# Optimization experiments

Hardware: AMD Instinct MI355X
Metric: run time of the kernel (lower is better)

Reference implementation:

```python
import jax, jax.numpy as jnp
import numpy as np

NB_COMP, LAT_DIM, OUT_DIM, N = 16, 128, 512, 16384


def setup_inputs() -> dict:
    key = jax.random.key(0)
    ks = jax.random.split(key, 8)
    eps = jax.random.normal(ks[0], (N, LAT_DIM), dtype=jnp.float32)
    c = jax.random.randint(ks[1], (N,), 0, NB_COMP, dtype=jnp.int32)
    mu = jax.random.normal(ks[2], (NB_COMP, LAT_DIM), dtype=jnp.float32)
    sigma = jax.random.uniform(ks[3], (NB_COMP, LAT_DIM), dtype=jnp.float32)
    # Kaiming-ish init for the two expert linear layers
    W1 = jax.random.normal(ks[4], (NB_COMP, OUT_DIM, LAT_DIM), dtype=jnp.float32) / np.sqrt(LAT_DIM)
    b1 = jax.random.normal(ks[5], (NB_COMP, OUT_DIM), dtype=jnp.float32) * 0.01
    W2 = jax.random.normal(ks[6], (NB_COMP, OUT_DIM, OUT_DIM), dtype=jnp.float32) / np.sqrt(OUT_DIM)
    b2 = jax.random.normal(ks[7], (NB_COMP, OUT_DIM), dtype=jnp.float32) * 0.01
    return {"n": N, "eps": eps, "c": c, "mu": mu, "sigma": sigma,
            "W1": W1, "b1": b1, "W2": W2, "b2": b2}


def reference(n, eps, c, mu, sigma, W1, b1, W2, b2):
    # Per-sample latent from its component's mean-field variational dist:
    # lat[k] = eps[k] * sigma[c[k]] + mu[c[k]]
    lat = eps * sigma[c] + mu[c]                                  # (n, lat_dim)
    # Run every expert's 2-layer MLP densely, then select per-sample expert.
    hidden = jax.nn.relu(jnp.einsum("nd,chd->cnh", lat, W1) + b1[:, None, :])  # (C, n, H)
    out_all = jnp.einsum("cnh,cwh->cnw", hidden, W2) + b2[:, None, :]          # (C, n, W)
    return out_all[c, jnp.arange(n)]                              # (n, weights_dim)
```

## Files before the change

kernel.cpp:

```cpp
#include <hip/hip_runtime.h>

#define NB 16
#define LD 128
#define OD 512
#define NS 16384
#define NPMAX (NS + NB*128)
#define NMT (NPMAX/128)

typedef __attribute__((ext_vector_type(8))) short short8;
typedef __attribute__((ext_vector_type(4))) float f32x4;

#define WS_OFF     128
#define WS_POFF    256
#define WS_PERM    1024
#define WS_W1B     (128*1024)
#define WS_W2B     (WS_W1B + 2*1024*1024)
#define WS_HID     (WS_W2B + 8*1024*1024)
#define WS_LAT     (WS_HID + 20*1024*1024)

#define GLDS16(g, l) __builtin_amdgcn_global_load_lds( \
    (const __attribute__((address_space(1))) unsigned int*)(g), \
    (__attribute__((address_space(3))) unsigned int*)(l), 16, 0, 0)

static __device__ __forceinline__ unsigned short f2bf(float f) {
  unsigned int u = __float_as_uint(f);
  u += 0x7FFFu + ((u >> 16) & 1u);
  return (unsigned short)(u >> 16);
}

#define SORT_T 1024
#define SORT_CH (NS / SORT_T)
__global__ __launch_bounds__(SORT_T) void k_sort(
    const int* __restrict__ c, int* __restrict__ off, int* __restrict__ poff,
    int* __restrict__ perm) {
  __shared__ int cnt[NB * SORT_T];
  __shared__ int totals[NB];
  __shared__ int ebase[NB];

  const int t = threadIdx.x;
  for (int e = 0; e < NB; ++e) cnt[e * SORT_T + t] = 0;
  __syncthreads();

  int myc[SORT_CH];
  for (int i = 0; i < SORT_CH; ++i) {
    int e = c[t * SORT_CH + i];
    myc[i] = e;
    cnt[e * SORT_T + t]++;
  }
  __syncthreads();

  const int w = t >> 6, l = t & 63;
  {
    int carry = 0;
    for (int chunk = 0; chunk < SORT_T / 64; ++chunk) {
      int idx = chunk * 64 + l;
      int v0 = cnt[w * SORT_T + idx];
      int v = v0;
      for (int d = 1; d < 64; d <<= 1) {
        int n = __shfl_up(v, d);
        if (l >= d) v += n;
      }
      cnt[w * SORT_T + idx] = carry + (v - v0);
      carry += __shfl(v, 63);
    }
    if (l == 0) totals[w] = carry;
  }
  __syncthreads();

  if (t == 0) {
    int o = 0, p = 0;
    for (int e = 0; e < NB; ++e) {
      off[e] = o; poff[e] = p; ebase[e] = o;
      o += totals[e];
      p += ((totals[e] + 127) >> 7) << 7;
    }
    off[NB] = o; poff[NB] = p;
  }
  __syncthreads();

  for (int i = 0; i < SORT_CH; ++i) {
    int e = myc[i];
    int pos = ebase[e] + cnt[e * SORT_T + t]++;
    perm[pos] = t * SORT_CH + i;
  }
}

__global__ void k_conv(const float* __restrict__ W1, const float* __restrict__ W2,
                       unsigned short* __restrict__ W1b, unsigned short* __restrict__ W2b) {
  const int n1 = NB * OD * LD / 4, n2 = NB * OD * OD / 4;
  for (int i = blockIdx.x * blockDim.x + threadIdx.x; i < n1 + n2;
       i += gridDim.x * blockDim.x) {
    float4 v; unsigned short* dst;
    if (i < n1) { v = ((const float4*)W1)[i]; dst = W1b + (size_t)i * 4; }
    else        { v = ((const float4*)W2)[i - n1]; dst = W2b + (size_t)(i - n1) * 4; }
    ushort4 o = make_ushort4(f2bf(v.x), f2bf(v.y), f2bf(v.z), f2bf(v.w));
    *(ushort4*)dst = o;
  }
}

__global__ __launch_bounds__(256) void k_lat(
    const float* __restrict__ eps, const float* __restrict__ mu,
    const float* __restrict__ sigma,
    const int* __restrict__ off, const int* __restrict__ poff,
    const int* __restrict__ perm, unsigned short* __restrict__ lat) {
  const int p0 = blockIdx.x * 8;
  if (p0 >= poff[NB]) return;
  int e = 0;
  while (e < NB - 1 && poff[e + 1] <= p0) e++;
  const int off_e = off[e], cnt = off[e + 1] - off_e;
  const int t = threadIdx.x;
  const int p = p0 + (t >> 5), col = (t & 31) * 4;
  const int lrow = p - poff[e];
  ushort4 o;
  if (lrow < cnt) {
    int src = perm[off_e + lrow];
    float4 v  = *(const float4*)(eps + (size_t)src * LD + col);
    float4 sg = *(const float4*)(sigma + e * LD + col);
    float4 m  = *(const float4*)(mu + e * LD + col);
    o = make_ushort4(f2bf(v.x * sg.x + m.x), f2bf(v.y * sg.y + m.y),
                     f2bf(v.z * sg.z + m.z), f2bf(v.w * sg.w + m.w));
  } else {
    o = make_ushort4(0, 0, 0, 0);
  }
  *(ushort4*)(lat + (size_t)p * LD + col) = o;
}

__global__ __launch_bounds__(256) void k_gemm1(
    const float* __restrict__ b1, const unsigned short* __restrict__ W1b,
    const unsigned short* __restrict__ lat,
    const int* __restrict__ poff, unsigned short* __restrict__ hidden) {
  __shared__ alignas(16) unsigned short As[128 * 64];
  __shared__ alignas(16) unsigned short Bs[128 * 64];

  const int mt = blockIdx.y, ct = blockIdx.x;
  const int pr0 = mt * 128;
  if (pr0 >= poff[NB]) return;
  int e = 0;
  while (e < NB - 1 && poff[e + 1] <= pr0) e++;

  const int t = threadIdx.x, w = t >> 6, lane = t & 63;
  const int wr = w >> 1, wc = w & 1;
  const int fr = lane & 15, fg = lane >> 4;
  const int srow = lane >> 3, scol = (lane & 7) * 8;

  f32x4 acc[4][4] = {};
  for (int kt = 0; kt < 2; ++kt) {
#pragma unroll
    for (int i = 0; i < 4; ++i) {
      const int ci = w * 4 + i;
      const int row = ci * 8 + srow;
      GLDS16(lat + (size_t)(pr0 + row) * LD + kt * 64 + scol, As + ci * 512);
      GLDS16(W1b + ((size_t)e * OD + ct * 128 + row) * LD + kt * 64 + scol, Bs + ci * 512);
    }
    __syncthreads();
#pragma unroll
    for (int ks = 0; ks < 2; ++ks) {
      short8 a[4], b[4];
#pragma unroll
      for (int fm = 0; fm < 4; ++fm)
        a[fm] = *(const short8*)(As + (wr * 64 + fm * 16 + fr) * 64 + ks * 32 + fg * 8);
#pragma unroll
      for (int fn = 0; fn < 4; ++fn)
        b[fn] = *(const short8*)(Bs + (wc * 64 + fn * 16 + fr) * 64 + ks * 32 + fg * 8);
#pragma unroll
      for (int fm = 0; fm < 4; ++fm)
#pragma unroll
        for (int fn = 0; fn < 4; ++fn)
          acc[fm][fn] = __builtin_amdgcn_mfma_f32_16x16x32_bf16(a[fm], b[fn], acc[fm][fn], 0, 0, 0);
    }
    __syncthreads();
  }

  const int colb = ct * 128 + wc * 64;
  float bias[4];
#pragma unroll
  for (int fn = 0; fn < 4; ++fn) bias[fn] = b1[e * OD + colb + fn * 16 + fr];
#pragma unroll
  for (int fm = 0; fm < 4; ++fm) {
    const int row0 = pr0 + wr * 64 + fm * 16 + fg * 4;
#pragma unroll
    for (int j = 0; j < 4; ++j) {
      unsigned short* hrow = hidden + (size_t)(row0 + j) * OD + colb;
#pragma unroll
      for (int fn = 0; fn < 4; ++fn)
        hrow[fn * 16 + fr] = f2bf(fmaxf(acc[fm][fn][j] + bias[fn], 0.f));
    }
  }
}

__global__ __launch_bounds__(256) void k_gemm2(
    const float* __restrict__ b2, const unsigned short* __restrict__ W2b,
    const unsigned short* __restrict__ hidden,
    const int* __restrict__ off, const int* __restrict__ poff,
    const int* __restrict__ perm, float* __restrict__ out) {
  __shared__ alignas(16) unsigned short As[128 * 64];
  __shared__ alignas(16) unsigned short Bs[128 * 64];

  const int mt = blockIdx.y, ct = blockIdx.x;
  const int pr0 = mt * 128;
  if (pr0 >= poff[NB]) return;
  int e = 0;
  while (e < NB - 1 && poff[e + 1] <= pr0) e++;
  const int off_e = off[e];
  const int cnt   = off[e + 1] - off_e;
  const int l0    = pr0 - poff[e];

  const int t = threadIdx.x, w = t >> 6, lane = t & 63;
  const int wr = w >> 1, wc = w & 1;
  const int fr = lane & 15, fg = lane >> 4;
  const int srow = lane >> 3, scol = (lane & 7) * 8;

  f32x4 acc[4][4] = {};
  for (int kt = 0; kt < 8; ++kt) {
#pragma unroll
    for (int i = 0; i < 4; ++i) {
      const int ci = w * 4 + i;
      const int row = ci * 8 + srow;
      GLDS16(hidden + (size_t)(pr0 + row) * OD + kt * 64 + scol, As + ci * 512);
      GLDS16(W2b + ((size_t)e * OD + ct * 128 + row) * OD + kt * 64 + scol, Bs + ci * 512);
    }
    __syncthreads();
#pragma unroll
    for (int ks = 0; ks < 2; ++ks) {
      short8 a[4], b[4];
#pragma unroll
      for (int fm = 0; fm < 4; ++fm)
        a[fm] = *(const short8*)(As + (wr * 64 + fm * 16 + fr) * 64 + ks * 32 + fg * 8);
#pragma unroll
      for (int fn = 0; fn < 4; ++fn)
        b[fn] = *(const short8*)(Bs + (wc * 64 + fn * 16 + fr) * 64 + ks * 32 + fg * 8);
#pragma unroll
      for (int fm = 0; fm < 4; ++fm)
#pragma unroll
        for (int fn = 0; fn < 4; ++fn)
          acc[fm][fn] = __builtin_amdgcn_mfma_f32_16x16x32_bf16(a[fm], b[fn], acc[fm][fn], 0, 0, 0);
    }
    __syncthreads();
  }

  const int colb = ct * 128 + wc * 64;
  float bias[4];
#pragma unroll
  for (int fn = 0; fn < 4; ++fn) bias[fn] = b2[e * OD + colb + fn * 16 + fr];
#pragma unroll
  for (int fm = 0; fm < 4; ++fm) {
    const int rl0 = wr * 64 + fm * 16 + fg * 4;
#pragma unroll
    for (int j = 0; j < 4; ++j) {
      const int lr = l0 + rl0 + j;
      if (lr < cnt) {
        const int k = perm[off_e + lr];
        float* orow = out + (size_t)k * OD + colb;
#pragma unroll
        for (int fn = 0; fn < 4; ++fn)
          orow[fn * 16 + fr] = acc[fm][fn][j] + bias[fn];
      }
    }
  }
}

extern "C" void kernel_launch(void* const* d_in, const int* in_sizes, int n_in,
                              void* d_out, int out_size, void* d_ws, size_t ws_size,
                              hipStream_t stream) {
  const float* eps   = (const float*)d_in[1];
  const int*   c     = (const int*)d_in[2];
  const float* mu    = (const float*)d_in[3];
  const float* sigma = (const float*)d_in[4];
  const float* W1    = (const float*)d_in[5];
  const float* b1    = (const float*)d_in[6];
  const float* W2    = (const float*)d_in[7];
  const float* b2    = (const float*)d_in[8];
  float* out = (float*)d_out;
  char*  ws  = (char*)d_ws;

  int* off     = (int*)(ws + WS_OFF);
  int* poff    = (int*)(ws + WS_POFF);
  int* perm    = (int*)(ws + WS_PERM);
  unsigned short* W1b = (unsigned short*)(ws + WS_W1B);
  unsigned short* W2b = (unsigned short*)(ws + WS_W2B);
  unsigned short* hid = (unsigned short*)(ws + WS_HID);
  unsigned short* lat = (unsigned short*)(ws + WS_LAT);

  k_conv<<<2048, 256, 0, stream>>>(W1, W2, W1b, W2b);
  k_sort<<<1, SORT_T, 0, stream>>>(c, off, poff, perm);
  k_lat<<<NPMAX / 8, 256, 0, stream>>>(eps, mu, sigma, off, poff, perm, lat);
  k_gemm1<<<dim3(4, NMT), 256, 0, stream>>>(b1, W1b, lat, poff, hid);
  k_gemm2<<<dim3(4, NMT), 256, 0, stream>>>(b2, W2b, hid, off, poff, perm, out);
}
```

Baseline: 71.69 us.

## Fuse weight conversion with sort and swizzle block order across XCDs

Merges the single-block sort and the bf16 weight conversion into one launch: block 0 sorts while the remaining blocks convert weights, which overlaps the serial sort with the bandwidth-bound conversion and removes one launch. The lat and GEMM kernels now use 1D grids whose block index is remapped so that consecutive logical tiles land on the same XCD (stride 8), aiming for better L2 locality of shared expert weights. The remap relies on hard-coded grid sizes (2304, 576) matching NPMAX. The sort block now uses 1024 threads and the whole 16K×4-byte LDS allocation, so conversion blocks also reserve that LDS, which can lower their occupancy.

```diff
diff --git a/kernel.cpp b/kernel.cpp
--- a/kernel.cpp
+++ b/kernel.cpp
@@ -30,71 +30,72 @@
 
 #define SORT_T 1024
 #define SORT_CH (NS / SORT_T)
-__global__ __launch_bounds__(SORT_T) void k_sort(
-    const int* __restrict__ c, int* __restrict__ off, int* __restrict__ poff,
-    int* __restrict__ perm) {
+__global__ __launch_bounds__(SORT_T) void k_convsort(
+    const float* __restrict__ W1, const float* __restrict__ W2,
+    const int* __restrict__ c,
+    unsigned short* __restrict__ W1b, unsigned short* __restrict__ W2b,
+    int* __restrict__ off, int* __restrict__ poff, int* __restrict__ perm) {
   __shared__ int cnt[NB * SORT_T];
   __shared__ int totals[NB];
   __shared__ int ebase[NB];
 
   const int t = threadIdx.x;
-  for (int e = 0; e < NB; ++e) cnt[e * SORT_T + t] = 0;
-  __syncthreads();
-
-  int myc[SORT_CH];
-  for (int i = 0; i < SORT_CH; ++i) {
-    int e = c[t * SORT_CH + i];
-    myc[i] = e;
-    cnt[e * SORT_T + t]++;
-  }
-  __syncthreads();
-
-  const int w = t >> 6, l = t & 63;
-  {
-    int carry = 0;
-    for (int chunk = 0; chunk < SORT_T / 64; ++chunk) {
-      int idx = chunk * 64 + l;
-      int v0 = cnt[w * SORT_T + idx];
-      int v = v0;
-      for (int d = 1; d < 64; d <<= 1) {
-        int n = __shfl_up(v, d);
-        if (l >= d) v += n;
+  if (blockIdx.x == 0) {
+    for (int e = 0; e < NB; ++e) cnt[e * SORT_T + t] = 0;
+    __syncthreads();
+
+    int myc[SORT_CH];
+    for (int i = 0; i < SORT_CH; ++i) {
+      int e = c[t * SORT_CH + i];
+      myc[i] = e;
+      cnt[e * SORT_T + t]++;
+    }
+    __syncthreads();
+
+    const int w = t >> 6, l = t & 63;
+    {
+      int carry = 0;
+      for (int chunk = 0; chunk < SORT_T / 64; ++chunk) {
+        int idx = chunk * 64 + l;
+        int v0 = cnt[w * SORT_T + idx];
+        int v = v0;
+        for (int d = 1; d < 64; d <<= 1) {
+          int n = __shfl_up(v, d);
+          if (l >= d) v += n;
+        }
+        cnt[w * SORT_T + idx] = carry + (v - v0);
+        carry += __shfl(v, 63);
       }
-      cnt[w * SORT_T + idx] = carry + (v - v0);
-      carry += __shfl(v, 63);
-    }
-    if (l == 0) totals[w] = carry;
-  }
-  __syncthreads();
-
-  if (t == 0) {
-    int o = 0, p = 0;
-    for (int e = 0; e < NB; ++e) {
-      off[e] = o; poff[e] = p; ebase[e] = o;
-      o += totals[e];
-      p += ((totals[e] + 127) >> 7) << 7;
-    }
-    off[NB] = o; poff[NB] = p;
-  }
-  __syncthreads();
-
-  for (int i = 0; i < SORT_CH; ++i) {
-    int e = myc[i];
-    int pos = ebase[e] + cnt[e * SORT_T + t]++;
-    perm[pos] = t * SORT_CH + i;
-  }
-}
-
-__global__ void k_conv(const float* __restrict__ W1, const float* __restrict__ W2,
-                       unsigned short* __restrict__ W1b, unsigned short* __restrict__ W2b) {
-  const int n1 = NB * OD * LD / 4, n2 = NB * OD * OD / 4;
-  for (int i = blockIdx.x * blockDim.x + threadIdx.x; i < n1 + n2;
-       i += gridDim.x * blockDim.x) {
-    float4 v; unsigned short* dst;
-    if (i < n1) { v = ((const float4*)W1)[i]; dst = W1b + (size_t)i * 4; }
-    else        { v = ((const float4*)W2)[i - n1]; dst = W2b + (size_t)(i - n1) * 4; }
-    ushort4 o = make_ushort4(f2bf(v.x), f2bf(v.y), f2bf(v.z), f2bf(v.w));
-    *(ushort4*)dst = o;
+      if (l == 0) totals[w] = carry;
+    }
+    __syncthreads();
+
+    if (t == 0) {
+      int o = 0, p = 0;
+      for (int e = 0; e < NB; ++e) {
+        off[e] = o; poff[e] = p; ebase[e] = o;
+        o += totals[e];
+        p += ((totals[e] + 127) >> 7) << 7;
+      }
+      off[NB] = o; poff[NB] = p;
+    }
+    __syncthreads();
+
+    for (int i = 0; i < SORT_CH; ++i) {
+      int e = myc[i];
+      int pos = ebase[e] + cnt[e * SORT_T + t]++;
+      perm[pos] = t * SORT_CH + i;
+    }
+  } else {
+    const int n1 = NB * OD * LD / 4, n2 = NB * OD * OD / 4;
+    for (int i = (blockIdx.x - 1) * SORT_T + t; i < n1 + n2;
+         i += (gridDim.x - 1) * SORT_T) {
+      float4 v; unsigned short* dst;
+      if (i < n1) { v = ((const float4*)W1)[i]; dst = W1b + (size_t)i * 4; }
+      else        { v = ((const float4*)W2)[i - n1]; dst = W2b + (size_t)(i - n1) * 4; }
+      ushort4 o = make_ushort4(f2bf(v.x), f2bf(v.y), f2bf(v.z), f2bf(v.w));
+      *(ushort4*)dst = o;
+    }
   }
 }
 
@@ -103,7 +104,9 @@
     const float* __restrict__ sigma,
     const int* __restrict__ off, const int* __restrict__ poff,
     const int* __restrict__ perm, unsigned short* __restrict__ lat) {
-  const int p0 = blockIdx.x * 8;
+  const int L = blockIdx.x;
+  const int b = (L & 7) * 288 + (L >> 3);
+  const int p0 = b * 8;
   if (p0 >= poff[NB]) return;
   int e = 0;
   while (e < NB - 1 && poff[e + 1] <= p0) e++;
@@ -132,7 +135,9 @@
   __shared__ alignas(16) unsigned short As[128 * 64];
   __shared__ alignas(16) unsigned short Bs[128 * 64];
 
-  const int mt = blockIdx.y, ct = blockIdx.x;
+  const int L = blockIdx.x;
+  const int s = (L & 7) * 72 + (L >> 3);
+  const int mt = s >> 2, ct = s & 3;
   const int pr0 = mt * 128;
   if (pr0 >= poff[NB]) return;
   int e = 0;
@@ -196,7 +201,9 @@
   __shared__ alignas(16) unsigned short As[128 * 64];
   __shared__ alignas(16) unsigned short Bs[128 * 64];
 
-  const int mt = blockIdx.y, ct = blockIdx.x;
+  const int L = blockIdx.x;
+  const int s = (L & 7) * 72 + (L >> 3);
+  const int mt = s >> 2, ct = s & 3;
   const int pr0 = mt * 128;
   if (pr0 >= poff[NB]) return;
   int e = 0;
@@ -281,9 +288,8 @@
   unsigned short* hid = (unsigned short*)(ws + WS_HID);
   unsigned short* lat = (unsigned short*)(ws + WS_LAT);
 
-  k_conv<<<2048, 256, 0, stream>>>(W1, W2, W1b, W2b);
-  k_sort<<<1, SORT_T, 0, stream>>>(c, off, poff, perm);
-  k_lat<<<NPMAX / 8, 256, 0, stream>>>(eps, mu, sigma, off, poff, perm, lat);
-  k_gemm1<<<dim3(4, NMT), 256, 0, stream>>>(b1, W1b, lat, poff, hid);
-  k_gemm2<<<dim3(4, NMT), 256, 0, stream>>>(b2, W2b, hid, off, poff, perm, out);
-}
+  k_convsort<<<512, SORT_T, 0, stream>>>(W1, W2, c, W1b, W2b, off, poff, perm);
+  k_lat<<<2304, 256, 0, stream>>>(eps, mu, sigma, off, poff, perm, lat);
+  k_gemm1<<<576, 256, 0, stream>>>(b1, W1b, lat, poff, hid);
+  k_gemm2<<<576, 256, 0, stream>>>(b2, W2b, hid, off, poff, perm, out);
+}
```

After: 66.56 us (median of 2 runs). 7.2% less time.
